# Kernel optimization log

Measured on AMD Instinct MI355X. Metric: run time of the kernel, lower is better.

## Reference

```python
import jax, jax.numpy as jnp
import numpy as np

N = 50000      # nodes
E = 800000     # edges (before self loops)
IN = 128       # in_ch
HID = 128      # hid (conv1 concat output)
OUT = 128      # out_ch
H = 4          # heads in conv1
NEG_SLOPE = 0.2


def setup_inputs() -> dict:
    key = jax.random.key(0)
    ks = jax.random.split(key, 16)
    s = 0.05
    return {
        "x": jax.random.normal(ks[0], (N, IN), dtype=jnp.float32),
        "edge_index": jax.random.randint(ks[1], (2, E), 0, N, dtype=jnp.int64),
        # conv1 params (heads=4, per-head dim HID//H)
        "W1l": jax.random.normal(ks[2], (IN, HID), dtype=jnp.float32) * s,
        "b1l": jnp.zeros((HID,), jnp.float32),
        "W1r": jax.random.normal(ks[3], (IN, HID), dtype=jnp.float32) * s,
        "b1r": jnp.zeros((HID,), jnp.float32),
        "att1": jax.random.normal(ks[4], (H, HID // H), dtype=jnp.float32) * s,
        "bias1": jnp.zeros((HID,), jnp.float32),
        # conv2 params (heads=1)
        "W2l": jax.random.normal(ks[5], (HID, OUT), dtype=jnp.float32) * s,
        "b2l": jnp.zeros((OUT,), jnp.float32),
        "W2r": jax.random.normal(ks[6], (HID, OUT), dtype=jnp.float32) * s,
        "b2r": jnp.zeros((OUT,), jnp.float32),
        "att2": jax.random.normal(ks[7], (1, OUT), dtype=jnp.float32) * s,
        "bias2": jnp.zeros((OUT,), jnp.float32),
    }


def gatv2_conv(x, src, dst, Wl, bl, Wr, br, att, heads):
    """PyG GATv2Conv (share_weights=False, concat=True).
    message(j->i): e = LeakyReLU(x_l[j] + x_r[i]); logit = <e, att>;
    softmax over edges per destination i; out_i = sum alpha * x_l[j].
    """
    n = x.shape[0]
    c = Wl.shape[1] // heads
    xl = (x @ Wl + bl).reshape(n, heads, c)   # source transform
    xr = (x @ Wr + br).reshape(n, heads, c)   # destination transform
    e = jax.nn.leaky_relu(xl[src] + xr[dst], NEG_SLOPE)      # [E, H, C]
    logits = jnp.einsum("ehc,hc->eh", e, att)                 # [E, H]
    m = jax.lax.stop_gradient(
        jax.ops.segment_max(logits, dst, num_segments=n))     # [N, H]
    p = jnp.exp(logits - m[dst])                              # [E, H]
    denom = jax.ops.segment_sum(p, dst, num_segments=n)       # [N, H]
    alpha = p / denom[dst]                                    # [E, H]
    out = jax.ops.segment_sum(xl[src] * alpha[..., None], dst,
                              num_segments=n)                 # [N, H, C]
    return out.reshape(n, heads * c)


def reference(x, edge_index, W1l, b1l, W1r, b1r, att1, bias1,
              W2l, b2l, W2r, b2r, att2, bias2):
    n = x.shape[0]
    # PyG default add_self_loops=True
    loops = jnp.arange(n, dtype=edge_index.dtype)
    src = jnp.concatenate([edge_index[0], loops])
    dst = jnp.concatenate([edge_index[1], loops])
    h = gatv2_conv(x, src, dst, W1l, b1l, W1r, b1r, att1, H) + bias1
    h = jax.nn.relu(h)
    out = gatv2_conv(h, src, dst, W2l, b2l, W2r, b2r, att2, 1) + bias2
    return out
```

## Files before the change

### kernel.cpp

```cpp
#include <hip/hip_runtime.h>
#include <hip/hip_bf16.h>

#define NODES 50000
#define NEDGE 800000
#define CH 128
#define NEG_SLOPE 0.2f
#define SCAN_CHUNK 2048
#define NBLK ((NODES + SCAN_CHUNK - 1) / SCAN_CHUNK)
#define NINF -1.0e30f
#define LOG2E 1.44269504088896340736f
#define RESCALE_THR 8.0f
#define NSLICE 400
#define SSLICE (NEDGE / NSLICE)
#define ZB ((NODES + 255) / 256)
#define GR 64
#define GGC ((NODES + GR - 1) / GR)
#define LDP 136

typedef short short8 __attribute__((ext_vector_type(8)));
typedef float f32x4 __attribute__((ext_vector_type(4)));
typedef float f32x2 __attribute__((ext_vector_type(2)));

__device__ __forceinline__ unsigned fbits(float f) {
    union { float f; unsigned u; } v; v.f = f; return v.u;
}
__device__ __forceinline__ float asf(unsigned u) {
    union { float f; unsigned u; } v; v.u = u; return v.f;
}
__device__ __forceinline__ unsigned short f2bf(float f) {
    unsigned u = fbits(f);
    unsigned r = u + 0x7fff + ((u >> 16) & 1);
    return (unsigned short)(r >> 16);
}
__device__ __forceinline__ float bf2f(unsigned short h) {
    return asf(((unsigned)h) << 16);
}
__device__ __forceinline__ void bf8cvt2(uint4 u, f32x2* f) {
    f[0] = (f32x2){asf(u.x << 16), asf(u.x & 0xFFFF0000u)};
    f[1] = (f32x2){asf(u.y << 16), asf(u.y & 0xFFFF0000u)};
    f[2] = (f32x2){asf(u.z << 16), asf(u.z & 0xFFFF0000u)};
    f[3] = (f32x2){asf(u.w << 16), asf(u.w & 0xFFFF0000u)};
}
__device__ __forceinline__ int dset(int dst) {
    return (int)(((unsigned)dst * 8u) / 50000u);
}

__global__ __launch_bounds__(256) void prep_kernel(const void* idx, int* flag,
                                                   int* cnt,
                                                   const float* __restrict__ W0,
                                                   const float* __restrict__ W1,
                                                   const float* __restrict__ W2,
                                                   const float* __restrict__ W3,
                                                   unsigned short* __restrict__ wbase) {
    int b = (int)blockIdx.x;
    if (b < ZB) {
        int t = b * 256 + (int)threadIdx.x;
        if (t < NODES) cnt[t] = 0;
        if (b == 0 && threadIdx.x < 64) {
            const int* w = (const int*)idx;
            int nz = (w[2 * threadIdx.x + 1] != 0) ? 1 : 0;
            unsigned long long bal = __ballot(nz);
            if (threadIdx.x == 0) *flag = (bal == 0ull) ? 1 : 0;
        }
        return;
    }
    int wb = b - ZB;
    int which = wb >> 6;
    const float* W = (which == 0) ? W0 : (which == 1) ? W1 : (which == 2) ? W2 : W3;
    unsigned short* hiT = wbase + (size_t)which * 32768;
    unsigned short* loT = hiT + 16384;
    int i = (wb & 63) * 256 + (int)threadIdx.x;
    int k = i >> 7, n = i & 127;
    float f = W[i];
    unsigned short h = f2bf(f);
    unsigned short l = f2bf(f - bf2f(h));
    hiT[n * CH + k] = h;
    loT[n * CH + k] = l;
}

__global__ __launch_bounds__(256) void hist_part_kernel(const void* idx,
                                                        const int* flag,
                                                        int* cnt) {
    int set = blockIdx.x & 7;
    int slice = blockIdx.x >> 3;
    int base = slice * SSLICE;
    int endE = base + SSLICE;
    int i64 = *flag;
    const int* w = (const int*)idx;
    for (int e = base + (int)threadIdx.x; e < endE; e += 256) {
        int dst = i64 ? w[2 * (NEDGE + e)] : w[NEDGE + e];
        if (dset(dst) == set) atomicAdd(&cnt[dst], 1);
    }
}

__global__ __launch_bounds__(256) void scan1_kernel(const int* __restrict__ cnt,
                                                    int* __restrict__ bsum) {
    int base = blockIdx.x * SCAN_CHUNK + (int)threadIdx.x * 8;
    int s = 0;
    #pragma unroll
    for (int k = 0; k < 8; ++k) {
        int i = base + k;
        s += (i < NODES) ? cnt[i] : 0;
    }
    #pragma unroll
    for (int m = 1; m < 64; m <<= 1) s += __shfl_xor(s, m);
    __shared__ int ws[4];
    if ((threadIdx.x & 63) == 0) ws[threadIdx.x >> 6] = s;
    __syncthreads();
    if (threadIdx.x == 0) bsum[blockIdx.x] = ws[0] + ws[1] + ws[2] + ws[3];
}

__global__ __launch_bounds__(256) void scan3_kernel(const int* __restrict__ cnt,
                                                    const int* __restrict__ bsum,
                                                    int* __restrict__ offs,
                                                    int* __restrict__ cursor) {
    int tid = (int)threadIdx.x;
    int bpre = 0;
    #pragma unroll
    for (int b = 0; b < NBLK; ++b) bpre += (b < (int)blockIdx.x) ? bsum[b] : 0;

    int base = blockIdx.x * SCAN_CHUNK + tid * 8;
    int v[8];
    int s = 0;
    #pragma unroll
    for (int k = 0; k < 8; ++k) {
        int i = base + k;
        v[k] = (i < NODES) ? cnt[i] : 0;
        s += v[k];
    }
    int lane = tid & 63;
    int incl = s;
    #pragma unroll
    for (int m = 1; m < 64; m <<= 1) {
        int t = __shfl_up(incl, m);
        if (lane >= m) incl += t;
    }
    __shared__ int wtot[4];
    if (lane == 63) wtot[tid >> 6] = incl;
    __syncthreads();
    int w = tid >> 6;
    int wbase = 0;
    #pragma unroll
    for (int k = 0; k < 4; ++k) wbase += (k < w) ? wtot[k] : 0;
    int excl = bpre + wbase + (incl - s);
    #pragma unroll
    for (int k = 0; k < 8; ++k) {
        int i = base + k;
        if (i < NODES) { offs[i] = excl; cursor[i] = excl; }
        excl += v[k];
    }
    if (blockIdx.x == 0 && tid == 0) offs[NODES] = NEDGE;
}

__global__ __launch_bounds__(512) void gemm1_scatter(
        const float* __restrict__ X,
        const unsigned short* __restrict__ whTl, const unsigned short* __restrict__ wlTl,
        const unsigned short* __restrict__ whTr, const unsigned short* __restrict__ wlTr,
        const float* __restrict__ bl, const float* __restrict__ br,
        unsigned short* __restrict__ Ylb, float* __restrict__ Yr, int nrows,
        const void* idx, const int* flag, int* cursor, int* __restrict__ srcs) {
    __shared__ unsigned short xh[GR][LDP];
    __shared__ unsigned short xlo[GR][LDP];

    if (blockIdx.x >= GGC) {
        int set = (int)blockIdx.x & 7;
        int slice = ((int)blockIdx.x - GGC) >> 3;
        int base = slice * SSLICE;
        int endE = base + SSLICE;
        int i64 = *flag;
        const int* w = (const int*)idx;
        for (int e = base + (int)threadIdx.x; e < endE; e += 512) {
            int dst = i64 ? w[2 * (NEDGE + e)] : w[NEDGE + e];
            if (dset(dst) == set) {
                int src = i64 ? w[2 * e] : w[e];
                int pos = atomicAdd(&cursor[dst], 1);
                srcs[pos] = src;
            }
        }
        return;
    }

    int r0 = blockIdx.x * GR;
    int tid = (int)threadIdx.x;

    {
        int row = tid >> 3;
        int c0 = (tid & 7) * 16;
        const float* src = X + (size_t)(r0 + row) * CH + c0;
        bool valid = (r0 + row) < nrows;
        #pragma unroll
        for (int j = 0; j < 16; j += 4) {
            float4 v = valid ? *(const float4*)(src + j)
                             : make_float4(0.f, 0.f, 0.f, 0.f);
            unsigned ux = fbits(v.x), uy = fbits(v.y);
            unsigned uz = fbits(v.z), uw = fbits(v.w);
            unsigned hx = ux & 0xFFFF0000u, hy = uy & 0xFFFF0000u;
            unsigned hz = uz & 0xFFFF0000u, hw = uw & 0xFFFF0000u;
            uint2 hp;
            hp.x = (ux >> 16) | hy;
            hp.y = (uz >> 16) | hw;
            float lx = v.x - asf(hx), ly = v.y - asf(hy);
            float lz = v.z - asf(hz), lw = v.w - asf(hw);
            uint2 lp;
            lp.x = (fbits(lx) >> 16) | (fbits(ly) & 0xFFFF0000u);
            lp.y = (fbits(lz) >> 16) | (fbits(lw) & 0xFFFF0000u);
            *(uint2*)&xh[row][c0 + j]  = hp;
            *(uint2*)&xlo[row][c0 + j] = lp;
        }
    }
    __syncthreads();

    int wave = tid >> 6;
    int lane = tid & 63;
    int l15 = lane & 15, q = lane >> 4;

    f32x4 acc[4][2];
    #pragma unroll
    for (int mt = 0; mt < 4; ++mt)
        #pragma unroll
        for (int nt = 0; nt < 2; ++nt) acc[mt][nt] = (f32x4)0.f;

    const unsigned short* bhp[2];
    const unsigned short* blp_[2];
    int ncol[2];
    #pragma unroll
    for (int nt = 0; nt < 2; ++nt) {
        int n = (wave * 2 + nt) * 16 + l15;
        ncol[nt] = n;
        int nn = n & 127;
        bhp[nt]  = ((n < CH) ? whTl : whTr) + (size_t)nn * CH;
        blp_[nt] = ((n < CH) ? wlTl : wlTr) + (size_t)nn * CH;
    }

    for (int kt = 0; kt < 4; ++kt) {
        int kofs = kt * 32 + q * 8;
        short8 ah[4], al[4];
        #pragma unroll
        for (int mt = 0; mt < 4; ++mt) {
            ah[mt] = *(const short8*)&xh[mt * 16 + l15][kofs];
            al[mt] = *(const short8*)&xlo[mt * 16 + l15][kofs];
        }
        #pragma unroll
        for (int nt = 0; nt < 2; ++nt) {
            short8 bh8 = *(const short8*)(bhp[nt] + kofs);
            short8 bl8 = *(const short8*)(blp_[nt] + kofs);
            #pragma unroll
            for (int mt = 0; mt < 4; ++mt) {
                acc[mt][nt] = __builtin_amdgcn_mfma_f32_16x16x32_bf16(
                                  ah[mt], bh8, acc[mt][nt], 0, 0, 0);
                acc[mt][nt] = __builtin_amdgcn_mfma_f32_16x16x32_bf16(
                                  al[mt], bh8, acc[mt][nt], 0, 0, 0);
                acc[mt][nt] = __builtin_amdgcn_mfma_f32_16x16x32_bf16(
                                  ah[mt], bl8, acc[mt][nt], 0, 0, 0);
            }
        }
    }

    #pragma unroll
    for (int nt = 0; nt < 2; ++nt) {
        int n = ncol[nt];
        int nc = n & 127;
        if (n < CH) {
            float bv = bl[nc];
            #pragma unroll
            for (int mt = 0; mt < 4; ++mt)
                #pragma unroll
                for (int reg = 0; reg < 4; ++reg) {
                    int row = r0 + mt * 16 + q * 4 + reg;
                    if (row < nrows)
                        Ylb[(size_t)row * CH + nc] = f2bf(acc[mt][nt][reg] + bv);
                }
        } else {
            float bv = br[nc];
            #pragma unroll
            for (int mt = 0; mt < 4; ++mt)
                #pragma unroll
                for (int reg = 0; reg < 4; ++reg) {
                    int row = r0 + mt * 16 + q * 4 + reg;
                    if (row < nrows)
                        Yr[(size_t)row * CH + nc] = acc[mt][nt][reg] + bv;
                }
        }
    }
}

__global__ __launch_bounds__(512) void gemm_dual_mfma_pl(
        const unsigned short* __restrict__ Ah, const unsigned short* __restrict__ Al,
        const unsigned short* __restrict__ whTl, const unsigned short* __restrict__ wlTl,
        const unsigned short* __restrict__ whTr, const unsigned short* __restrict__ wlTr,
        const float* __restrict__ bl, const float* __restrict__ br,
        unsigned short* __restrict__ Ylb, float* __restrict__ Yr, int nrows) {
    __shared__ unsigned short xh[GR][LDP];
    __shared__ unsigned short xlo[GR][LDP];

    int r0 = blockIdx.x * GR;
    int tid = (int)threadIdx.x;

    {
        int row = tid >> 3;
        int c0 = (tid & 7) * 16;
        int gr = r0 + row;
        if (gr > nrows - 1) gr = nrows - 1;
        const uint4* ph = (const uint4*)(Ah + (size_t)gr * CH + c0);
        const uint4* pl = (const uint4*)(Al + (size_t)gr * CH + c0);
        uint4 h0 = ph[0], h1 = ph[1];
        uint4 l0 = pl[0], l1 = pl[1];
        *(uint4*)&xh[row][c0]      = h0;
        *(uint4*)&xh[row][c0 + 8]  = h1;
        *(uint4*)&xlo[row][c0]     = l0;
        *(uint4*)&xlo[row][c0 + 8] = l1;
    }
    __syncthreads();

    int wave = tid >> 6;
    int lane = tid & 63;
    int l15 = lane & 15, q = lane >> 4;

    f32x4 acc[4][2];
    #pragma unroll
    for (int mt = 0; mt < 4; ++mt)
        #pragma unroll
        for (int nt = 0; nt < 2; ++nt) acc[mt][nt] = (f32x4)0.f;

    const unsigned short* bhp[2];
    const unsigned short* blp_[2];
    int ncol[2];
    #pragma unroll
    for (int nt = 0; nt < 2; ++nt) {
        int n = (wave * 2 + nt) * 16 + l15;
        ncol[nt] = n;
        int nn = n & 127;
        bhp[nt]  = ((n < CH) ? whTl : whTr) + (size_t)nn * CH;
        blp_[nt] = ((n < CH) ? wlTl : wlTr) + (size_t)nn * CH;
    }

    for (int kt = 0; kt < 4; ++kt) {
        int kofs = kt * 32 + q * 8;
        short8 ah[4], al[4];
        #pragma unroll
        for (int mt = 0; mt < 4; ++mt) {
            ah[mt] = *(const short8*)&xh[mt * 16 + l15][kofs];
            al[mt] = *(const short8*)&xlo[mt * 16 + l15][kofs];
        }
        #pragma unroll
        for (int nt = 0; nt < 2; ++nt) {
            short8 bh8 = *(const short8*)(bhp[nt] + kofs);
            short8 bl8 = *(const short8*)(blp_[nt] + kofs);
            #pragma unroll
            for (int mt = 0; mt < 4; ++mt) {
                acc[mt][nt] = __builtin_amdgcn_mfma_f32_16x16x32_bf16(
                                  ah[mt], bh8, acc[mt][nt], 0, 0, 0);
                acc[mt][nt] = __builtin_amdgcn_mfma_f32_16x16x32_bf16(
                                  al[mt], bh8, acc[mt][nt], 0, 0, 0);
                acc[mt][nt] = __builtin_amdgcn_mfma_f32_16x16x32_bf16(
                                  ah[mt], bl8, acc[mt][nt], 0, 0, 0);
            }
        }
    }

    #pragma unroll
    for (int nt = 0; nt < 2; ++nt) {
        int n = ncol[nt];
        int nc = n & 127;
        if (n < CH) {
            float bv = bl[nc];
            #pragma unroll
            for (int mt = 0; mt < 4; ++mt)
                #pragma unroll
                for (int reg = 0; reg < 4; ++reg) {
                    int row = r0 + mt * 16 + q * 4 + reg;
                    if (row < nrows)
                        Ylb[(size_t)row * CH + nc] = f2bf(acc[mt][nt][reg] + bv);
                }
        } else {
            float bv = br[nc];
            #pragma unroll
            for (int mt = 0; mt < 4; ++mt)
                #pragma unroll
                for (int reg = 0; reg < 4; ++reg) {
                    int row = r0 + mt * 16 + q * 4 + reg;
                    if (row < nrows)
                        Yr[(size_t)row * CH + nc] = acc[mt][nt][reg] + bv;
                }
        }
    }
}

template <int HEADS, bool RELU, bool SPLITOUT>
__global__ __launch_bounds__(256) void node_pass(
        const unsigned short* __restrict__ xlb,
        const float* __restrict__ xr,
        const float* __restrict__ att,
        const float* __restrict__ bias,
        const int* __restrict__ offs, const int* __restrict__ srcs,
        float* __restrict__ outf,
        unsigned short* __restrict__ outh, unsigned short* __restrict__ outl) {
    constexpr int GL = (CH / HEADS) / 8;
    int wave = (int)threadIdx.x >> 6;
    int i = blockIdx.x * 4 + wave;
    int lane = (int)threadIdx.x & 63;
    int g = lane >> 4;
    int l16 = lane & 15;
    int c0 = l16 * 8;

    f32x2 r2[4], a2[4], s2[4];
    {
        const float4* xrp = (const float4*)(xr + (size_t)i * CH + c0);
        float4 r0 = xrp[0], r1 = xrp[1];
        r2[0] = (f32x2){r0.x, r0.y}; r2[1] = (f32x2){r0.z, r0.w};
        r2[2] = (f32x2){r1.x, r1.y}; r2[3] = (f32x2){r1.z, r1.w};
        const float4* atp = (const float4*)(att + c0);
        float4 a0 = atp[0], a1 = atp[1];
        a2[0] = (f32x2){a0.x, a0.y} * LOG2E; a2[1] = (f32x2){a0.z, a0.w} * LOG2E;
        a2[2] = (f32x2){a1.x, a1.y} * LOG2E; a2[3] = (f32x2){a1.z, a1.w} * LOG2E;
    }
    uint4 us = *(const uint4*)(xlb + (size_t)i * CH + c0);
    bf8cvt2(us, s2);

    f32x2 td = (f32x2)0.f;
    #pragma unroll
    for (int k = 0; k < 4; ++k) {
        f32x2 z = s2[k] + r2[k];
        f32x2 l = __builtin_elementwise_max(z, z * NEG_SLOPE);
        td += l * a2[k];
    }
    float ts = td.x + td.y;
    #pragma unroll
    for (int msk = 1; msk < GL; msk <<= 1) ts += __shfl_xor(ts, msk);

    float m = ts;
    float d = (g == 0) ? 1.f : 0.f;
    f32x2 acc2[4];
    #pragma unroll
    for (int k = 0; k < 4; ++k) acc2[k] = (g == 0) ? s2[k] : (f32x2)0.f;

    int beg = offs[i], end = offs[i + 1];
    int deg = end - beg;
    int iters = (deg + 3) >> 2;
    if (iters > 0) {
        int last = end - 1;
        int e = beg + g;
        int si = srcs[min(e, last)];
        uint4 u = *(const uint4*)(xlb + (size_t)si * CH + c0);

        for (int it = 0; it < iters; ++it, e += 4) {
            bool valid = e < end;
            int sn = srcs[min(e + 4, last)];
            uint4 un = *(const uint4*)(xlb + (size_t)sn * CH + c0);

            f32x2 f2[4];
            bf8cvt2(u, f2);
            f32x2 td2 = (f32x2)0.f;
            #pragma unroll
            for (int k = 0; k < 4; ++k) {
                f32x2 z = f2[k] + r2[k];
                f32x2 l = __builtin_elementwise_max(z, z * NEG_SLOPE);
                td2 += l * a2[k];
            }
            float t = td2.x + td2.y;
            #pragma unroll
            for (int msk = 1; msk < GL; msk <<= 1) t += __shfl_xor(t, msk);
            t = valid ? t : NINF;

            if (__any(t > m + RESCALE_THR)) {
                float nm = fmaxf(m, t);
                float sc = exp2f(m - nm);
                float p  = exp2f(t - nm);
                d = d * sc + p;
                #pragma unroll
                for (int k = 0; k < 4; ++k) acc2[k] = acc2[k] * sc + f2[k] * p;
                m = nm;
            } else {
                float p = exp2f(t - m);
                d += p;
                #pragma unroll
                for (int k = 0; k < 4; ++k) acc2[k] += f2[k] * p;
            }
            u = un;
        }
    }

    #pragma unroll
    for (int msk = 16; msk <= 32; msk <<= 1) {
        float mo  = __shfl_xor(m, msk);
        float dof = __shfl_xor(d, msk);
        float nm = fmaxf(m, mo);
        float s0 = exp2f(m - nm), s1 = exp2f(mo - nm);
        d = d * s0 + dof * s1;
        #pragma unroll
        for (int k = 0; k < 4; ++k) {
            f32x2 ao;
            ao.x = __shfl_xor(acc2[k].x, msk);
            ao.y = __shfl_xor(acc2[k].y, msk);
            acc2[k] = acc2[k] * s0 + ao * s1;
        }
        m = nm;
    }

    if (g == 0) {
        float inv = 1.0f / d;
        const float4* bp = (const float4*)(bias + c0);
        float4 b0 = bp[0], b1 = bp[1];
        float bb[8] = {b0.x, b0.y, b0.z, b0.w, b1.x, b1.y, b1.z, b1.w};
        float o[8];
        #pragma unroll
        for (int k = 0; k < 4; ++k) {
            o[2*k]   = acc2[k].x * inv + bb[2*k];
            o[2*k+1] = acc2[k].y * inv + bb[2*k+1];
        }
        #pragma unroll
        for (int c = 0; c < 8; ++c)
            if (RELU) o[c] = fmaxf(o[c], 0.f);
        if (SPLITOUT) {
            unsigned hu[8];
            float lo[8];
            #pragma unroll
            for (int c = 0; c < 8; ++c) {
                hu[c] = fbits(o[c]) & 0xFFFF0000u;
                lo[c] = o[c] - asf(hu[c]);
            }
            uint4 ph, pl;
            ph.x = (hu[0] >> 16) | hu[1];  ph.y = (hu[2] >> 16) | hu[3];
            ph.z = (hu[4] >> 16) | hu[5];  ph.w = (hu[6] >> 16) | hu[7];
            pl.x = (fbits(lo[0]) >> 16) | (fbits(lo[1]) & 0xFFFF0000u);
            pl.y = (fbits(lo[2]) >> 16) | (fbits(lo[3]) & 0xFFFF0000u);
            pl.z = (fbits(lo[4]) >> 16) | (fbits(lo[5]) & 0xFFFF0000u);
            pl.w = (fbits(lo[6]) >> 16) | (fbits(lo[7]) & 0xFFFF0000u);
            *(uint4*)(outh + (size_t)i * CH + c0) = ph;
            *(uint4*)(outl + (size_t)i * CH + c0) = pl;
        } else {
            float4 w0 = make_float4(o[0], o[1], o[2], o[3]);
            float4 w1 = make_float4(o[4], o[5], o[6], o[7]);
            float4* op = (float4*)(outf + (size_t)i * CH + c0);
            op[0] = w0; op[1] = w1;
        }
    }
}

extern "C" void kernel_launch(void* const* d_in, const int* in_sizes, int n_in,
                              void* d_out, int out_size, void* d_ws, size_t ws_size,
                              hipStream_t stream) {
    const float* x     = (const float*)d_in[0];
    const void*  eidx  = d_in[1];
    const float* W1l   = (const float*)d_in[2];
    const float* b1l   = (const float*)d_in[3];
    const float* W1r   = (const float*)d_in[4];
    const float* b1r   = (const float*)d_in[5];
    const float* att1  = (const float*)d_in[6];
    const float* bias1 = (const float*)d_in[7];
    const float* W2l   = (const float*)d_in[8];
    const float* b2l   = (const float*)d_in[9];
    const float* W2r   = (const float*)d_in[10];
    const float* b2r   = (const float*)d_in[11];
    const float* att2  = (const float*)d_in[12];
    const float* bias2 = (const float*)d_in[13];
    float* out = (float*)d_out;

    unsigned short* xlb = (unsigned short*)d_ws;
    float* xr = (float*)(xlb + (size_t)NODES * CH);
    unsigned short* hbh = (unsigned short*)(xr + (size_t)NODES * CH);
    unsigned short* hbl = hbh + (size_t)NODES * CH;
    int* offs   = (int*)(hbl + (size_t)NODES * CH);
    int* cnt    = offs + (NODES + 1);
    int* cursor = cnt + NODES;
    int* srcs   = cursor + NODES;
    int* flag   = srcs + NEDGE;
    int* bsum   = flag + 1;
    unsigned short* wbuf =
        (unsigned short*)(((uintptr_t)(bsum + NBLK) + 15) & ~(uintptr_t)15);
    unsigned short* w1lh = wbuf;              unsigned short* w1ll = wbuf + 16384;
    unsigned short* w1rh = wbuf + 32768;      unsigned short* w1rl = wbuf + 49152;
    unsigned short* w2lh = wbuf + 65536;      unsigned short* w2ll = wbuf + 81920;
    unsigned short* w2rh = wbuf + 98304;      unsigned short* w2rl = wbuf + 114688;

    const int PG = NSLICE * 8;
    const int FG = GGC + NSLICE * 8;

    prep_kernel<<<ZB + 256, 256, 0, stream>>>(eidx, flag, cnt,
                                              W1l, W1r, W2l, W2r, wbuf);
    hist_part_kernel<<<PG, 256, 0, stream>>>(eidx, flag, cnt);
    scan1_kernel<<<NBLK, 256, 0, stream>>>(cnt, bsum);
    scan3_kernel<<<NBLK, 256, 0, stream>>>(cnt, bsum, offs, cursor);

    gemm1_scatter<<<FG, 512, 0, stream>>>(x, w1lh, w1ll, w1rh, w1rl,
                                          b1l, b1r, xlb, xr, NODES,
                                          eidx, flag, cursor, srcs);

    node_pass<4, true, true><<<(NODES + 3) / 4, 256, 0, stream>>>(
        xlb, xr, att1, bias1, offs, srcs, nullptr, hbh, hbl);

    gemm_dual_mfma_pl<<<GGC, 512, 0, stream>>>(hbh, hbl, w2lh, w2ll, w2rh, w2rl,
                                               b2l, b2r, xlb, xr, NODES);
    node_pass<1, false, false><<<(NODES + 3) / 4, 256, 0, stream>>>(
        xlb, xr, att2, bias2, offs, srcs, out, nullptr, nullptr);
}
```

Baseline: 326.9 us.

## Split first-layer GEMM across histogram and scatter kernels to overlap work

The layer-1 projection GEMM is split into two halves. The first half runs in the same launch as the destination-degree histogram, and the second half runs alongside the CSR scatter. The standalone histogram kernel is removed. The aim is to fill idle compute units during the atomic-bound histogram and scatter phases, at the cost of larger histogram slices and different block scheduling.

Measured after the change: 322.1 us (median of 2 runs). About the same (-1.5%).

```diff
diff --git a/kernel.cpp b/kernel.cpp
--- a/kernel.cpp
+++ b/kernel.cpp
@@ -12,9 +12,13 @@
 #define RESCALE_THR 8.0f
 #define NSLICE 400
 #define SSLICE (NEDGE / NSLICE)
+#define HSLICE 4000
+#define NHS (NEDGE / HSLICE)
 #define ZB ((NODES + 255) / 256)
 #define GR 64
 #define GGC ((NODES + GR - 1) / GR)
+#define GB 391
+#define HROWS (GB * GR)
 #define LDP 136
 
 typedef short short8 __attribute__((ext_vector_type(8)));
@@ -78,21 +82,6 @@
     loT[n * CH + k] = l;
 }
 
-__global__ __launch_bounds__(256) void hist_part_kernel(const void* idx,
-                                                        const int* flag,
-                                                        int* cnt) {
-    int set = blockIdx.x & 7;
-    int slice = blockIdx.x >> 3;
-    int base = slice * SSLICE;
-    int endE = base + SSLICE;
-    int i64 = *flag;
-    const int* w = (const int*)idx;
-    for (int e = base + (int)threadIdx.x; e < endE; e += 256) {
-        int dst = i64 ? w[2 * (NEDGE + e)] : w[NEDGE + e];
-        if (dset(dst) == set) atomicAdd(&cnt[dst], 1);
-    }
-}
-
 __global__ __launch_bounds__(256) void scan1_kernel(const int* __restrict__ cnt,
                                                     int* __restrict__ bsum) {
     int base = blockIdx.x * SCAN_CHUNK + (int)threadIdx.x * 8;
@@ -152,37 +141,14 @@
     if (blockIdx.x == 0 && tid == 0) offs[NODES] = NEDGE;
 }
 
-__global__ __launch_bounds__(512) void gemm1_scatter(
+__device__ __forceinline__ void gemm1_role(
+        int r0, int tid,
+        unsigned short (*xh)[LDP], unsigned short (*xlo)[LDP],
         const float* __restrict__ X,
         const unsigned short* __restrict__ whTl, const unsigned short* __restrict__ wlTl,
         const unsigned short* __restrict__ whTr, const unsigned short* __restrict__ wlTr,
         const float* __restrict__ bl, const float* __restrict__ br,
-        unsigned short* __restrict__ Ylb, float* __restrict__ Yr, int nrows,
-        const void* idx, const int* flag, int* cursor, int* __restrict__ srcs) {
-    __shared__ unsigned short xh[GR][LDP];
-    __shared__ unsigned short xlo[GR][LDP];
-
-    if (blockIdx.x >= GGC) {
-        int set = (int)blockIdx.x & 7;
-        int slice = ((int)blockIdx.x - GGC) >> 3;
-        int base = slice * SSLICE;
-        int endE = base + SSLICE;
-        int i64 = *flag;
-        const int* w = (const int*)idx;
-        for (int e = base + (int)threadIdx.x; e < endE; e += 512) {
-            int dst = i64 ? w[2 * (NEDGE + e)] : w[NEDGE + e];
-            if (dset(dst) == set) {
-                int src = i64 ? w[2 * e] : w[e];
-                int pos = atomicAdd(&cursor[dst], 1);
-                srcs[pos] = src;
-            }
-        }
-        return;
-    }
-
-    int r0 = blockIdx.x * GR;
-    int tid = (int)threadIdx.x;
-
+        unsigned short* __restrict__ Ylb, float* __restrict__ Yr, int nrows) {
     {
         int row = tid >> 3;
         int c0 = (tid & 7) * 16;
@@ -282,6 +248,64 @@
                 }
         }
     }
+}
+
+__global__ __launch_bounds__(512) void gemm1a_hist(
+        const float* __restrict__ X,
+        const unsigned short* __restrict__ whTl, const unsigned short* __restrict__ wlTl,
+        const unsigned short* __restrict__ whTr, const unsigned short* __restrict__ wlTr,
+        const float* __restrict__ bl, const float* __restrict__ br,
+        unsigned short* __restrict__ Ylb, float* __restrict__ Yr, int nrows,
+        const void* idx, const int* flag, int* cnt) {
+    __shared__ unsigned short xh[GR][LDP];
+    __shared__ unsigned short xlo[GR][LDP];
+
+    if (blockIdx.x >= GB) {
+        int set = (int)blockIdx.x & 7;
+        int slice = ((int)blockIdx.x - GB) >> 3;
+        int base = slice * HSLICE;
+        int endE = base + HSLICE;
+        int i64 = *flag;
+        const int* w = (const int*)idx;
+        for (int e = base + (int)threadIdx.x; e < endE; e += 512) {
+            int dst = i64 ? w[2 * (NEDGE + e)] : w[NEDGE + e];
+            if (dset(dst) == set) atomicAdd(&cnt[dst], 1);
+        }
+        return;
+    }
+    gemm1_role(blockIdx.x * GR, (int)threadIdx.x, xh, xlo,
+               X, whTl, wlTl, whTr, wlTr, bl, br, Ylb, Yr, nrows);
+}
+
+__global__ __launch_bounds__(512) void gemm1b_scatter(
+        const float* __restrict__ X,
+        const unsigned short* __restrict__ whTl, const unsigned short* __restrict__ wlTl,
+        const unsigned short* __restrict__ whTr, const unsigned short* __restrict__ wlTr,
+        const float* __restrict__ bl, const float* __restrict__ br,
+        unsigned short* __restrict__ Ylb, float* __restrict__ Yr, int nrows,
+        const void* idx, const int* flag, int* cursor, int* __restrict__ srcs) {
+    __shared__ unsigned short xh[GR][LDP];
+    __shared__ unsigned short xlo[GR][LDP];
+
+    if (blockIdx.x >= GB) {
+        int set = (int)blockIdx.x & 7;
+        int slice = ((int)blockIdx.x - GB) >> 3;
+        int base = slice * SSLICE;
+        int endE = base + SSLICE;
+        int i64 = *flag;
+        const int* w = (const int*)idx;
+        for (int e = base + (int)threadIdx.x; e < endE; e += 512) {
+            int dst = i64 ? w[2 * (NEDGE + e)] : w[NEDGE + e];
+            if (dset(dst) == set) {
+                int src = i64 ? w[2 * e] : w[e];
+                int pos = atomicAdd(&cursor[dst], 1);
+                srcs[pos] = src;
+            }
+        }
+        return;
+    }
+    gemm1_role(HROWS + blockIdx.x * GR, (int)threadIdx.x, xh, xlo,
+               X, whTl, wlTl, whTr, wlTr, bl, br, Ylb, Yr, nrows);
 }
 
 __global__ __launch_bounds__(512) void gemm_dual_mfma_pl(
@@ -573,18 +597,22 @@
     unsigned short* w2lh = wbuf + 65536;      unsigned short* w2ll = wbuf + 81920;
     unsigned short* w2rh = wbuf + 98304;      unsigned short* w2rl = wbuf + 114688;
 
-    const int PG = NSLICE * 8;
-    const int FG = GGC + NSLICE * 8;
+    const int FGA = GB + NHS * 8;
+    const int FGB = GB + NSLICE * 8;
 
     prep_kernel<<<ZB + 256, 256, 0, stream>>>(eidx, flag, cnt,
                                               W1l, W1r, W2l, W2r, wbuf);
-    hist_part_kernel<<<PG, 256, 0, stream>>>(eidx, flag, cnt);
+
+    gemm1a_hist<<<FGA, 512, 0, stream>>>(x, w1lh, w1ll, w1rh, w1rl,
+                                         b1l, b1r, xlb, xr, NODES,
+                                         eidx, flag, cnt);
+
     scan1_kernel<<<NBLK, 256, 0, stream>>>(cnt, bsum);
     scan3_kernel<<<NBLK, 256, 0, stream>>>(cnt, bsum, offs, cursor);
 
-    gemm1_scatter<<<FG, 512, 0, stream>>>(x, w1lh, w1ll, w1rh, w1rl,
-                                          b1l, b1r, xlb, xr, NODES,
-                                          eidx, flag, cursor, srcs);
+    gemm1b_scatter<<<FGB, 512, 0, stream>>>(x, w1lh, w1ll, w1rh, w1rl,
+                                            b1l, b1r, xlb, xr, NODES,
+                                            eidx, flag, cursor, srcs);
 
     node_pass<4, true, true><<<(NODES + 3) / 4, 256, 0, stream>>>(
         xlb, xr, att1, bias1, offs, srcs, nullptr, hbh, hbl);
```
